# Kernel optimization log

Hardware: AMD Instinct MI355X
Metric: run time of the kernel (lower is better)

The kernel has to match this reference:

```python
import jax, jax.numpy as jnp
import numpy as np

B, HW, NTGT, C = 2, 4096, 4096, 512
H, KNN = 8, 32
DH = C // H
SCALE = DH ** -0.5


def setup_inputs() -> dict:
    key = jax.random.key(0)
    ks = jax.random.split(key, 12)
    s = 1.0 / np.sqrt(C)
    return {
        "src": jax.random.normal(ks[0], (B, HW, C), jnp.float32),
        "tgt": jax.random.normal(ks[1], (B, NTGT, C), jnp.float32),
        "indices": jax.random.randint(ks[2], (B, HW, KNN), 0, NTGT, jnp.int64),
        "weights": jax.random.normal(ks[3], (B, HW, KNN), jnp.float32),
        "Wq": jax.random.normal(ks[4], (C, C), jnp.float32) * s,
        "bq": jnp.zeros((C,), jnp.float32),
        "Wk": jax.random.normal(ks[5], (C, C), jnp.float32) * s,
        "bk": jnp.zeros((C,), jnp.float32),
        "Wv": jax.random.normal(ks[6], (C, C), jnp.float32) * s,
        "bv": jnp.zeros((C,), jnp.float32),
        "Wo": jax.random.normal(ks[7], (C, C), jnp.float32) * s,
        "bo": jnp.zeros((C,), jnp.float32),
    }


def reference(src, tgt, indices, weights, Wq, bq, Wk, bk, Wv, bv, Wo, bo):
    b, hw, c = src.shape
    # projections -> (b, H, seq, dh)
    q = (src @ Wq + bq).reshape(b, hw, H, DH).transpose(0, 2, 1, 3)
    k = (tgt @ Wk + bk).reshape(b, -1, H, DH).transpose(0, 2, 1, 3)
    v = (tgt @ Wv + bv).reshape(b, -1, H, DH).transpose(0, 2, 1, 3)
    # gather epipolar neighbors: per batch, kb[:, idx] -> (H, hw, KNN, dh)
    gather = jax.vmap(lambda xb, ib: xb[:, ib])
    k_g = gather(k, indices)  # (b, H, hw, KNN, dh)
    v_g = gather(v, indices)  # (b, H, hw, KNN, dh)
    logits = jnp.einsum("bhqd,bhqkd->bhqk", q, k_g) * SCALE
    logits = logits + weights[:, None]  # broadcast over heads
    attn = jax.nn.softmax(logits, axis=-1)
    out = jnp.einsum("bhqk,bhqkd->bhqd", attn, v_g)
    out = out.transpose(0, 2, 1, 3).reshape(b, hw, c)
    return out @ Wo + bo
```

## Files before the change

kernel.cpp:

```cpp
#include <hip/hip_runtime.h>
#include <hip/hip_bf16.h>
#include <stdint.h>
#include <type_traits>

#define B_    2
#define HW_   4096
#define NTGT_ 4096
#define C_    512
#define H_    8
#define KNN_  32
#define DH_   64
#define M_    (B_ * HW_)

typedef unsigned short ushort_t;
typedef __bf16 bf16x8 __attribute__((ext_vector_type(8)));
typedef float floatx4 __attribute__((ext_vector_type(4)));

__device__ __forceinline__ float b2f(ushort_t u) {
    union { uint32_t i; float f; } x;
    x.i = ((uint32_t)u) << 16;
    return x.f;
}
__device__ __forceinline__ ushort_t f2b(float f) {
    union { float f; uint32_t i; } x;
    x.f = f;
    uint32_t r = x.i + 0x7fffu + ((x.i >> 16) & 1u);
    return (ushort_t)(r >> 16);
}
__device__ __forceinline__ uint32_t pk2(float x, float y) {
    union { __hip_bfloat162 h2; uint32_t u; } c;
    c.h2 = __float22bfloat162_rn(make_float2(x, y));
    return c.u;
}
__device__ __forceinline__ uint4 pack8(const float4& a, const float4& b) {
    return make_uint4(pk2(a.x, a.y), pk2(a.z, a.w), pk2(b.x, b.y), pk2(b.z, b.w));
}

__global__ __launch_bounds__(256) void transpose_cvt4(
    const float* __restrict__ W0, const float* __restrict__ W1,
    const float* __restrict__ W2, const float* __restrict__ W3,
    ushort_t* __restrict__ T0, ushort_t* __restrict__ T1,
    ushort_t* __restrict__ T2, ushort_t* __restrict__ T3) {
    __shared__ float tile[32][33];

    const float* W = (blockIdx.z == 0) ? W0 : (blockIdx.z == 1) ? W1
                     : (blockIdx.z == 2) ? W2 : W3;
    ushort_t* T = (blockIdx.z == 0) ? T0 : (blockIdx.z == 1) ? T1
                  : (blockIdx.z == 2) ? T2 : T3;

    const int k0 = blockIdx.x * 32;
    const int n0 = blockIdx.y * 32;
    const int t = threadIdx.x;
    const int r = t >> 3;
    const int c0 = (t & 7) * 4;

    float4 d = *(const float4*)&W[(size_t)(k0 + r) * 512 + n0 + c0];
    tile[r][c0 + 0] = d.x; tile[r][c0 + 1] = d.y;
    tile[r][c0 + 2] = d.z; tile[r][c0 + 3] = d.w;
    __syncthreads();

    uint2 o;
    o.x = pk2(tile[c0 + 0][r], tile[c0 + 1][r]);
    o.y = pk2(tile[c0 + 2][r], tile[c0 + 3][r]);
    *(uint2*)&T[(size_t)(n0 + r) * 512 + k0 + c0] = o;
}

__global__ __launch_bounds__(256) void transpose_inplace4_f32(
    float* W0, float* W1, float* W2, float* W3) {
    __shared__ float ta[32][33];
    __shared__ float tb[32][33];

    float* W = (blockIdx.y == 0) ? W0 : (blockIdx.y == 1) ? W1
               : (blockIdx.y == 2) ? W2 : W3;

    int p = blockIdx.x;
    int i = 0, acc = 0;
    while (acc + (16 - i) <= p) { acc += 16 - i; ++i; }
    const int j = i + (p - acc);

    const int t = threadIdx.x;
    const int r = t >> 3;
    const int c0 = (t & 7) * 4;

    {
        float4 d = *(const float4*)&W[(size_t)(i * 32 + r) * 512 + j * 32 + c0];
        ta[r][c0 + 0] = d.x; ta[r][c0 + 1] = d.y;
        ta[r][c0 + 2] = d.z; ta[r][c0 + 3] = d.w;
    }
    if (i != j) {
        float4 d = *(const float4*)&W[(size_t)(j * 32 + r) * 512 + i * 32 + c0];
        tb[r][c0 + 0] = d.x; tb[r][c0 + 1] = d.y;
        tb[r][c0 + 2] = d.z; tb[r][c0 + 3] = d.w;
    }
    __syncthreads();

    *(float4*)&W[(size_t)(j * 32 + r) * 512 + i * 32 + c0] =
        make_float4(ta[c0 + 0][r], ta[c0 + 1][r], ta[c0 + 2][r], ta[c0 + 3][r]);
    if (i != j)
        *(float4*)&W[(size_t)(i * 32 + r) * 512 + j * 32 + c0] =
            make_float4(tb[c0 + 0][r], tb[c0 + 1][r], tb[c0 + 2][r], tb[c0 + 3][r]);
}

template <typename AT, typename BT, typename OT, int BN>
__device__ __forceinline__ void gemm_body(const AT* __restrict__ A,
                                          const BT* __restrict__ Wt,
                                          const float* __restrict__ bias,
                                          OT* __restrict__ O,
                                          int bm, int bn) {
    constexpr int NJ = BN / 32;
    __shared__ ushort_t As[128][40];
    __shared__ ushort_t Bs[BN][40];

    const int t = threadIdx.x;
    const int lr = t >> 2;
    const int lc = (t & 3) * 8;

    const int lane = t & 63;
    const int wv = t >> 6;
    const int wr = (wv >> 1) * 64;
    const int wc = (wv & 1) * (BN / 2);
    const int r16 = lane & 15;
    const int quad = lane >> 4;

    floatx4 acc[4][NJ] = {};

    float4 fa0, fa1, fa2, fa3, fb0, fb1, fb2, fb3;
    uint4 ua0, ua1, ub0, ub1;

    if constexpr (std::is_same<AT, float>::value) {
        const float* p0 = &A[(size_t)(bm + lr) * 512 + lc];
        const float* p1 = &A[(size_t)(bm + lr + 64) * 512 + lc];
        fa0 = *(const float4*)p0; fa1 = *(const float4*)(p0 + 4);
        fa2 = *(const float4*)p1; fa3 = *(const float4*)(p1 + 4);
    } else {
        ua0 = *(const uint4*)&A[(size_t)(bm + lr) * 512 + lc];
        ua1 = *(const uint4*)&A[(size_t)(bm + lr + 64) * 512 + lc];
    }
    if constexpr (std::is_same<BT, float>::value) {
        const float* p0 = &Wt[(size_t)(bn + lr) * 512 + lc];
        fb0 = *(const float4*)p0; fb1 = *(const float4*)(p0 + 4);
        if constexpr (BN == 128) {
            const float* p1 = &Wt[(size_t)(bn + lr + 64) * 512 + lc];
            fb2 = *(const float4*)p1; fb3 = *(const float4*)(p1 + 4);
        }
    } else {
        ub0 = *(const uint4*)&Wt[(size_t)(bn + lr) * 512 + lc];
        if constexpr (BN == 128)
            ub1 = *(const uint4*)&Wt[(size_t)(bn + lr + 64) * 512 + lc];
    }

    for (int kt = 0; kt < 512; kt += 32) {
        __syncthreads();
        if constexpr (std::is_same<AT, float>::value) {
            *(uint4*)&As[lr][lc] = pack8(fa0, fa1);
            *(uint4*)&As[lr + 64][lc] = pack8(fa2, fa3);
        } else {
            *(uint4*)&As[lr][lc] = ua0;
            *(uint4*)&As[lr + 64][lc] = ua1;
        }
        if constexpr (std::is_same<BT, float>::value) {
            *(uint4*)&Bs[lr][lc] = pack8(fb0, fb1);
            if constexpr (BN == 128) *(uint4*)&Bs[lr + 64][lc] = pack8(fb2, fb3);
        } else {
            *(uint4*)&Bs[lr][lc] = ub0;
            if constexpr (BN == 128) *(uint4*)&Bs[lr + 64][lc] = ub1;
        }
        __syncthreads();

        if (kt + 32 < 512) {
            const int k2 = kt + 32;
            if constexpr (std::is_same<AT, float>::value) {
                const float* p0 = &A[(size_t)(bm + lr) * 512 + k2 + lc];
                const float* p1 = &A[(size_t)(bm + lr + 64) * 512 + k2 + lc];
                fa0 = *(const float4*)p0; fa1 = *(const float4*)(p0 + 4);
                fa2 = *(const float4*)p1; fa3 = *(const float4*)(p1 + 4);
            } else {
                ua0 = *(const uint4*)&A[(size_t)(bm + lr) * 512 + k2 + lc];
                ua1 = *(const uint4*)&A[(size_t)(bm + lr + 64) * 512 + k2 + lc];
            }
            if constexpr (std::is_same<BT, float>::value) {
                const float* p0 = &Wt[(size_t)(bn + lr) * 512 + k2 + lc];
                fb0 = *(const float4*)p0; fb1 = *(const float4*)(p0 + 4);
                if constexpr (BN == 128) {
                    const float* p1 = &Wt[(size_t)(bn + lr + 64) * 512 + k2 + lc];
                    fb2 = *(const float4*)p1; fb3 = *(const float4*)(p1 + 4);
                }
            } else {
                ub0 = *(const uint4*)&Wt[(size_t)(bn + lr) * 512 + k2 + lc];
                if constexpr (BN == 128)
                    ub1 = *(const uint4*)&Wt[(size_t)(bn + lr + 64) * 512 + k2 + lc];
            }
        }

        bf16x8 af[4], bf[NJ];
#pragma unroll
        for (int i = 0; i < 4; ++i)
            af[i] = *(const bf16x8*)&As[wr + i * 16 + r16][quad * 8];
#pragma unroll
        for (int j = 0; j < NJ; ++j)
            bf[j] = *(const bf16x8*)&Bs[wc + j * 16 + r16][quad * 8];
#pragma unroll
        for (int i = 0; i < 4; ++i)
#pragma unroll
            for (int j = 0; j < NJ; ++j)
                acc[i][j] = __builtin_amdgcn_mfma_f32_16x16x32_bf16(
                    af[i], bf[j], acc[i][j], 0, 0, 0);
    }

#pragma unroll
    for (int j = 0; j < NJ; ++j) {
        const int col = bn + wc + j * 16 + r16;
        const float bj = bias[col];
#pragma unroll
        for (int i = 0; i < 4; ++i) {
            const int row = bm + wr + i * 16 + quad * 4;
#pragma unroll
            for (int r = 0; r < 4; ++r) {
                float v = acc[i][j][r] + bj;
                if constexpr (std::is_same<OT, ushort_t>::value)
                    O[(size_t)(row + r) * 512 + col] = f2b(v);
                else
                    O[(size_t)(row + r) * 512 + col] = v;
            }
        }
    }
}

template <typename BT>
__global__ __launch_bounds__(256, 3) void gemm_qkv(
    const float* __restrict__ src, const float* __restrict__ tgt,
    const BT* __restrict__ WtQ, const BT* __restrict__ WtK,
    const BT* __restrict__ WtV,
    const float* __restrict__ bq, const float* __restrict__ bk,
    const float* __restrict__ bv,
    ushort_t* __restrict__ Qb, ushort_t* __restrict__ Kb,
    ushort_t* __restrict__ Vb) {
    const int id = blockIdx.x;
    const int xcd = id & 7;
    const int g = id >> 3;
    const int mgrp = g / 12;
    const int r = g % 12;
    const int z = r >> 2;
    const int bn = (r & 3) * 128;
    const int bm = (xcd + 8 * mgrp) * 128;

    const float* A = (z == 0) ? src : tgt;
    const BT* Wt = (z == 0) ? WtQ : (z == 1) ? WtK : WtV;
    const float* bias = (z == 0) ? bq : (z == 1) ? bk : bv;
    ushort_t* O = (z == 0) ? Qb : (z == 1) ? Kb : Vb;
    gemm_body<float, BT, ushort_t, 128>(A, Wt, bias, O, bm, bn);
}

template <typename BT, typename OT>
__global__ __launch_bounds__(256, 4) void gemm_o(const ushort_t* __restrict__ A,
                                                 const BT* __restrict__ Wt,
                                                 const float* __restrict__ bias,
                                                 OT* __restrict__ O) {
    const int id = blockIdx.x;
    const int xcd = id & 7;
    const int g = id >> 3;
    const int mgrp = g >> 3;
    const int bn = (g & 7) * 64;
    const int bm = (xcd + 8 * mgrp) * 128;
    gemm_body<ushort_t, BT, OT, 64>(A, Wt, bias, O, bm, bn);
}

#define KVSTRIDE 520
template <typename IT>
__global__ __launch_bounds__(256) void attn_kernel(const ushort_t* Q,
                                                   const ushort_t* __restrict__ K,
                                                   const ushort_t* __restrict__ V,
                                                   const IT* __restrict__ idx,
                                                   const float* __restrict__ wts,
                                                   ushort_t* O) {
    __shared__ float qs[512];
    __shared__ ushort_t kvs[KNN_][KVSTRIDE];
    __shared__ float ps[H_][KNN_];
    __shared__ int idxs[KNN_];
    __shared__ float ws[KNN_];

    const int t = threadIdx.x;
    const int id = blockIdx.x;
    const int xcd = id & 7;
    const int slot = id >> 3;
    const int b = xcd >> 2;
    const int bq = b * HW_ + (xcd & 3) * 1024 + slot;
    const size_t qoff = (size_t)bq * C_;

    {
        uint32_t d = *(const uint32_t*)(Q + qoff + 2 * t);
        qs[2 * t + 0] = b2f((ushort_t)(d & 0xffffu));
        qs[2 * t + 1] = b2f((ushort_t)(d >> 16));
    }
    if (t < KNN_) {
        idxs[t] = (int)idx[(size_t)bq * KNN_ + t];
        ws[t] = wts[(size_t)bq * KNN_ + t];
    }
    __syncthreads();

    const int sr = t >> 3;
    const int sg = (t & 7) * 8;
    {
        const ushort_t* krow = K + ((size_t)(b * NTGT_ + idxs[sr])) * C_;
#pragma unroll
        for (int j = 0; j < 8; ++j)
            *(uint4*)&kvs[sr][sg + j * 64] = *(const uint4*)(krow + sg + j * 64);
    }
    __syncthreads();

    const int h = t >> 5;
    const int n = t & 31;
    const float* qh = qs + h * DH_;
    float dot = 0.f;
#pragma unroll
    for (int j = 0; j < 8; ++j) {
        uint4 kv = *(const uint4*)&kvs[n][h * DH_ + j * 8];
        const int d0 = j * 8;
        dot = fmaf(qh[d0 + 0], b2f((ushort_t)(kv.x & 0xffffu)), dot);
        dot = fmaf(qh[d0 + 1], b2f((ushort_t)(kv.x >> 16)), dot);
        dot = fmaf(qh[d0 + 2], b2f((ushort_t)(kv.y & 0xffffu)), dot);
        dot = fmaf(qh[d0 + 3], b2f((ushort_t)(kv.y >> 16)), dot);
        dot = fmaf(qh[d0 + 4], b2f((ushort_t)(kv.z & 0xffffu)), dot);
        dot = fmaf(qh[d0 + 5], b2f((ushort_t)(kv.z >> 16)), dot);
        dot = fmaf(qh[d0 + 6], b2f((ushort_t)(kv.w & 0xffffu)), dot);
        dot = fmaf(qh[d0 + 7], b2f((ushort_t)(kv.w >> 16)), dot);
    }
    float logit = dot * 0.125f + ws[n];

    float mx = logit;
#pragma unroll
    for (int o = 16; o > 0; o >>= 1) mx = fmaxf(mx, __shfl_xor(mx, o));
    float e = __expf(logit - mx);
    float s = e;
#pragma unroll
    for (int o = 16; o > 0; o >>= 1) s += __shfl_xor(s, o);
    ps[h][n] = e / s;
    __syncthreads();

    {
        const ushort_t* vrow = V + ((size_t)(b * NTGT_ + idxs[sr])) * C_;
#pragma unroll
        for (int j = 0; j < 8; ++j)
            *(uint4*)&kvs[sr][sg + j * 64] = *(const uint4*)(vrow + sg + j * 64);
    }
    __syncthreads();

    const int d2 = (t & 31) * 2;
    float a0 = 0.f, a1 = 0.f;
#pragma unroll 8
    for (int nn = 0; nn < KNN_; ++nn) {
        uint32_t vv = *(const uint32_t*)&kvs[nn][h * DH_ + d2];
        float p = ps[h][nn];
        a0 = fmaf(p, b2f((ushort_t)(vv & 0xffffu)), a0);
        a1 = fmaf(p, b2f((ushort_t)(vv >> 16)), a1);
    }
    *(uint32_t*)(O + qoff + h * DH_ + d2) = pk2(a0, a1);
}

static int elem_bytes(const void* p, size_t n, int dflt) {
    size_t sz = 0;
    hipError_t err = hipPointerGetAttribute(
        &sz, HIP_POINTER_ATTRIBUTE_RANGE_SIZE, (hipDeviceptr_t)(uintptr_t)p);
    if (err == hipSuccess && sz >= n && (sz % n) == 0) {
        size_t b = sz / n;
        if (b == 2 || b == 4 || b == 8) return (int)b;
    }
    return dflt;
}

extern "C" void kernel_launch(void* const* d_in, const int* in_sizes, int n_in,
                              void* d_out, int out_size, void* d_ws, size_t ws_size,
                              hipStream_t stream) {
    const float* src  = (const float*)d_in[0];
    const float* tgt  = (const float*)d_in[1];
    const void*  idxp = d_in[2];
    const float* wtp  = (const float*)d_in[3];
    float* Wq = (float*)d_in[4];  const float* bq = (const float*)d_in[5];
    float* Wk = (float*)d_in[6];  const float* bk = (const float*)d_in[7];
    float* Wv = (float*)d_in[8];  const float* bv = (const float*)d_in[9];
    float* Wo = (float*)d_in[10]; const float* bo = (const float*)d_in[11];

    const size_t NELEM = (size_t)M_ * C_;
    const size_t WELEM = (size_t)C_ * C_;
    const size_t NIDX  = (size_t)B_ * HW_ * KNN_;

    const int ib = elem_bytes(idxp, NIDX, 4);
    const int ob = elem_bytes(d_out, NELEM, 4);

    dim3 blk(256);

    ushort_t* Qb = (ushort_t*)d_ws;
    ushort_t* Kb = Qb + NELEM;
    ushort_t* Vb = (ushort_t*)d_out;
    ushort_t* Ob = Qb;

    const bool wfit = ws_size >= (2 * NELEM + 4 * WELEM) * sizeof(ushort_t);

    if (wfit) {
        ushort_t* T = Kb + NELEM;
        ushort_t* WtQ = T;
        ushort_t* WtK = T + WELEM;
        ushort_t* WtV = T + 2 * WELEM;
        ushort_t* WtO = T + 3 * WELEM;

        transpose_cvt4<<<dim3(16, 16, 4), blk, 0, stream>>>(
            Wq, Wk, Wv, Wo, WtQ, WtK, WtV, WtO);

        gemm_qkv<ushort_t><<<dim3(768), blk, 0, stream>>>(
            src, tgt, WtQ, WtK, WtV, bq, bk, bv, Qb, Kb, Vb);

        if (ib == 8)
            attn_kernel<long long><<<dim3(B_ * HW_), blk, 0, stream>>>(
                Qb, Kb, Vb, (const long long*)idxp, wtp, Ob);
        else
            attn_kernel<int><<<dim3(B_ * HW_), blk, 0, stream>>>(
                Qb, Kb, Vb, (const int*)idxp, wtp, Ob);

        if (ob == 2)
            gemm_o<ushort_t, ushort_t><<<dim3(512), blk, 0, stream>>>(
                Ob, WtO, bo, (ushort_t*)d_out);
        else
            gemm_o<ushort_t, float><<<dim3(512), blk, 0, stream>>>(
                Ob, WtO, bo, (float*)d_out);
    } else {
        transpose_inplace4_f32<<<dim3(136, 4), blk, 0, stream>>>(Wq, Wk, Wv, Wo);

        gemm_qkv<float><<<dim3(768), blk, 0, stream>>>(
            src, tgt, Wq, Wk, Wv, bq, bk, bv, Qb, Kb, Vb);

        if (ib == 8)
            attn_kernel<long long><<<dim3(B_ * HW_), blk, 0, stream>>>(
                Qb, Kb, Vb, (const long long*)idxp, wtp, Ob);
        else
            attn_kernel<int><<<dim3(B_ * HW_), blk, 0, stream>>>(
                Qb, Kb, Vb, (const int*)idxp, wtp, Ob);

        if (ob == 2)
            gemm_o<float, ushort_t><<<dim3(512), blk, 0, stream>>>(
                Ob, Wo, bo, (ushort_t*)d_out);
        else
            gemm_o<float, float><<<dim3(512), blk, 0, stream>>>(
                Ob, Wo, bo, (float*)d_out);
    }
}
```

Measured before the change: 188.2 us.

## Pipeline K/V gathers in 16-row chunks through registers to cut attention LDS

```diff
diff --git a/kernel.cpp b/kernel.cpp
--- a/kernel.cpp
+++ b/kernel.cpp
@@ -267,14 +267,14 @@
 
 #define KVSTRIDE 520
 template <typename IT>
-__global__ __launch_bounds__(256) void attn_kernel(const ushort_t* Q,
-                                                   const ushort_t* __restrict__ K,
-                                                   const ushort_t* __restrict__ V,
-                                                   const IT* __restrict__ idx,
-                                                   const float* __restrict__ wts,
-                                                   ushort_t* O) {
-    __shared__ float qs[512];
-    __shared__ ushort_t kvs[KNN_][KVSTRIDE];
+__global__ __launch_bounds__(256, 7) void attn_kernel(const ushort_t* Q,
+                                                      const ushort_t* __restrict__ K,
+                                                      const ushort_t* __restrict__ V,
+                                                      const IT* __restrict__ idx,
+                                                      const float* __restrict__ wts,
+                                                      ushort_t* O) {
+    __shared__ float qs[16][34];
+    __shared__ ushort_t kvs[16][KVSTRIDE];
     __shared__ float ps[H_][KNN_];
     __shared__ int idxs[KNN_];
     __shared__ float ws[KNN_];
@@ -289,8 +289,9 @@
 
     {
         uint32_t d = *(const uint32_t*)(Q + qoff + 2 * t);
-        qs[2 * t + 0] = b2f((ushort_t)(d & 0xffffu));
-        qs[2 * t + 1] = b2f((ushort_t)(d >> 16));
+        const int qr = t >> 4, qc = (t & 15) * 2;
+        qs[qr][qc + 0] = b2f((ushort_t)(d & 0xffffu));
+        qs[qr][qc + 1] = b2f((ushort_t)(d >> 16));
     }
     if (t < KNN_) {
         idxs[t] = (int)idx[(size_t)bq * KNN_ + t];
@@ -298,59 +299,126 @@
     }
     __syncthreads();
 
-    const int sr = t >> 3;
-    const int sg = (t & 7) * 8;
-    {
-        const ushort_t* krow = K + ((size_t)(b * NTGT_ + idxs[sr])) * C_;
-#pragma unroll
-        for (int j = 0; j < 8; ++j)
-            *(uint4*)&kvs[sr][sg + j * 64] = *(const uint4*)(krow + sg + j * 64);
+    const ushort_t* Kbase = K + (size_t)b * NTGT_ * C_;
+    const ushort_t* Vbase = V + (size_t)b * NTGT_ * C_;
+    const int prow = t >> 4;
+    const int pcol = (t & 15) * 8;
+
+    uint4 r0, r1, r2, r3;
+    {
+        const ushort_t* p = Kbase + (size_t)idxs[prow] * C_ + pcol;
+        r0 = *(const uint4*)(p);       r1 = *(const uint4*)(p + 128);
+        r2 = *(const uint4*)(p + 256); r3 = *(const uint4*)(p + 384);
+    }
+    *(uint4*)&kvs[prow][pcol + 0]   = r0;
+    *(uint4*)&kvs[prow][pcol + 128] = r1;
+    *(uint4*)&kvs[prow][pcol + 256] = r2;
+    *(uint4*)&kvs[prow][pcol + 384] = r3;
+    {
+        const ushort_t* p = Kbase + (size_t)idxs[prow + 16] * C_ + pcol;
+        r0 = *(const uint4*)(p);       r1 = *(const uint4*)(p + 128);
+        r2 = *(const uint4*)(p + 256); r3 = *(const uint4*)(p + 384);
     }
     __syncthreads();
 
     const int h = t >> 5;
-    const int n = t & 31;
-    const float* qh = qs + h * DH_;
-    float dot = 0.f;
-#pragma unroll
-    for (int j = 0; j < 8; ++j) {
-        uint4 kv = *(const uint4*)&kvs[n][h * DH_ + j * 8];
-        const int d0 = j * 8;
-        dot = fmaf(qh[d0 + 0], b2f((ushort_t)(kv.x & 0xffffu)), dot);
-        dot = fmaf(qh[d0 + 1], b2f((ushort_t)(kv.x >> 16)), dot);
-        dot = fmaf(qh[d0 + 2], b2f((ushort_t)(kv.y & 0xffffu)), dot);
-        dot = fmaf(qh[d0 + 3], b2f((ushort_t)(kv.y >> 16)), dot);
-        dot = fmaf(qh[d0 + 4], b2f((ushort_t)(kv.z & 0xffffu)), dot);
-        dot = fmaf(qh[d0 + 5], b2f((ushort_t)(kv.z >> 16)), dot);
-        dot = fmaf(qh[d0 + 6], b2f((ushort_t)(kv.w & 0xffffu)), dot);
-        dot = fmaf(qh[d0 + 7], b2f((ushort_t)(kv.w >> 16)), dot);
-    }
-    float logit = dot * 0.125f + ws[n];
-
-    float mx = logit;
-#pragma unroll
-    for (int o = 16; o > 0; o >>= 1) mx = fmaxf(mx, __shfl_xor(mx, o));
-    float e = __expf(logit - mx);
-    float s = e;
-#pragma unroll
-    for (int o = 16; o > 0; o >>= 1) s += __shfl_xor(s, o);
-    ps[h][n] = e / s;
-    __syncthreads();
-
-    {
-        const ushort_t* vrow = V + ((size_t)(b * NTGT_ + idxs[sr])) * C_;
-#pragma unroll
-        for (int j = 0; j < 8; ++j)
-            *(uint4*)&kvs[sr][sg + j * 64] = *(const uint4*)(vrow + sg + j * 64);
-    }
-    __syncthreads();
-
-    const int d2 = (t & 31) * 2;
+    const int l5 = t & 31;
+    const int nl = l5 & 15;
+    const int half = l5 >> 4;
+    const float* qh = qs[h * 2 + half];
+    const int koff = h * 64 + half * 32;
+
+    float l0, l1;
+    {
+        float dot = 0.f;
+#pragma unroll
+        for (int j = 0; j < 4; ++j) {
+            uint4 kv = *(const uint4*)&kvs[nl][koff + j * 8];
+            const int d0 = j * 8;
+            dot = fmaf(qh[d0 + 0], b2f((ushort_t)(kv.x & 0xffffu)), dot);
+            dot = fmaf(qh[d0 + 1], b2f((ushort_t)(kv.x >> 16)), dot);
+            dot = fmaf(qh[d0 + 2], b2f((ushort_t)(kv.y & 0xffffu)), dot);
+            dot = fmaf(qh[d0 + 3], b2f((ushort_t)(kv.y >> 16)), dot);
+            dot = fmaf(qh[d0 + 4], b2f((ushort_t)(kv.z & 0xffffu)), dot);
+            dot = fmaf(qh[d0 + 5], b2f((ushort_t)(kv.z >> 16)), dot);
+            dot = fmaf(qh[d0 + 6], b2f((ushort_t)(kv.w & 0xffffu)), dot);
+            dot = fmaf(qh[d0 + 7], b2f((ushort_t)(kv.w >> 16)), dot);
+        }
+        dot += __shfl_xor(dot, 16);
+        l0 = dot * 0.125f + ws[nl];
+    }
+    __syncthreads();
+    *(uint4*)&kvs[prow][pcol + 0]   = r0;
+    *(uint4*)&kvs[prow][pcol + 128] = r1;
+    *(uint4*)&kvs[prow][pcol + 256] = r2;
+    *(uint4*)&kvs[prow][pcol + 384] = r3;
+    {
+        const ushort_t* p = Vbase + (size_t)idxs[prow] * C_ + pcol;
+        r0 = *(const uint4*)(p);       r1 = *(const uint4*)(p + 128);
+        r2 = *(const uint4*)(p + 256); r3 = *(const uint4*)(p + 384);
+    }
+    __syncthreads();
+    {
+        float dot = 0.f;
+#pragma unroll
+        for (int j = 0; j < 4; ++j) {
+            uint4 kv = *(const uint4*)&kvs[nl][koff + j * 8];
+            const int d0 = j * 8;
+            dot = fmaf(qh[d0 + 0], b2f((ushort_t)(kv.x & 0xffffu)), dot);
+            dot = fmaf(qh[d0 + 1], b2f((ushort_t)(kv.x >> 16)), dot);
+            dot = fmaf(qh[d0 + 2], b2f((ushort_t)(kv.y & 0xffffu)), dot);
+            dot = fmaf(qh[d0 + 3], b2f((ushort_t)(kv.y >> 16)), dot);
+            dot = fmaf(qh[d0 + 4], b2f((ushort_t)(kv.z & 0xffffu)), dot);
+            dot = fmaf(qh[d0 + 5], b2f((ushort_t)(kv.z >> 16)), dot);
+            dot = fmaf(qh[d0 + 6], b2f((ushort_t)(kv.w & 0xffffu)), dot);
+            dot = fmaf(qh[d0 + 7], b2f((ushort_t)(kv.w >> 16)), dot);
+        }
+        dot += __shfl_xor(dot, 16);
+        l1 = dot * 0.125f + ws[nl + 16];
+    }
+    {
+        float m = fmaxf(l0, l1);
+#pragma unroll
+        for (int o = 16; o > 0; o >>= 1) m = fmaxf(m, __shfl_xor(m, o));
+        float e0 = __expf(l0 - m), e1 = __expf(l1 - m);
+        float s = e0 + e1;
+#pragma unroll
+        for (int o = 16; o > 0; o >>= 1) s += __shfl_xor(s, o);
+        const float inv = 2.0f / s;
+        ps[h][nl] = e0 * inv;
+        ps[h][nl + 16] = e1 * inv;
+    }
+    __syncthreads();
+    *(uint4*)&kvs[prow][pcol + 0]   = r0;
+    *(uint4*)&kvs[prow][pcol + 128] = r1;
+    *(uint4*)&kvs[prow][pcol + 256] = r2;
+    *(uint4*)&kvs[prow][pcol + 384] = r3;
+    {
+        const ushort_t* p = Vbase + (size_t)idxs[prow + 16] * C_ + pcol;
+        r0 = *(const uint4*)(p);       r1 = *(const uint4*)(p + 128);
+        r2 = *(const uint4*)(p + 256); r3 = *(const uint4*)(p + 384);
+    }
+    __syncthreads();
+
+    const int d2 = l5 * 2;
     float a0 = 0.f, a1 = 0.f;
-#pragma unroll 8
-    for (int nn = 0; nn < KNN_; ++nn) {
+#pragma unroll
+    for (int nn = 0; nn < 16; ++nn) {
         uint32_t vv = *(const uint32_t*)&kvs[nn][h * DH_ + d2];
         float p = ps[h][nn];
+        a0 = fmaf(p, b2f((ushort_t)(vv & 0xffffu)), a0);
+        a1 = fmaf(p, b2f((ushort_t)(vv >> 16)), a1);
+    }
+    __syncthreads();
+    *(uint4*)&kvs[prow][pcol + 0]   = r0;
+    *(uint4*)&kvs[prow][pcol + 128] = r1;
+    *(uint4*)&kvs[prow][pcol + 256] = r2;
+    *(uint4*)&kvs[prow][pcol + 384] = r3;
+    __syncthreads();
+#pragma unroll
+    for (int nn = 0; nn < 16; ++nn) {
+        uint32_t vv = *(const uint32_t*)&kvs[nn][h * DH_ + d2];
+        float p = ps[h][nn + 16];
         a0 = fmaf(p, b2f((ushort_t)(vv & 0xffffu)), a0);
         a1 = fmaf(p, b2f((ushort_t)(vv >> 16)), a1);
     }
```

New measurement: 184.0 us. 2.3% less time.
